# Kernel tuning notes

Hardware: AMD Instinct MI355X
Metric: run time of the kernel (lower is better)

## Reference

```python
import jax, jax.numpy as jnp
import numpy as np

NUM_HEADS = 8

def setup_inputs() -> dict:
    key = jax.random.key(0)
    ks = jax.random.split(key, 12)
    T, B, C, D = 2048, 4, 512, 512
    s = 1.0 / np.sqrt(C)
    return {
        "key_in": jax.random.normal(ks[0], (T, B, C), jnp.float32),
        "value_in": jax.random.normal(ks[1], (T, B, C), jnp.float32),
        "query_in": jax.random.normal(ks[2], (T, B, C), jnp.float32),
        "Wk": jax.random.normal(ks[3], (C, D), jnp.float32) * s,
        "bk": jax.random.normal(ks[4], (D,), jnp.float32) * 0.01,
        "Wv": jax.random.normal(ks[5], (C, D), jnp.float32) * s,
        "bv": jax.random.normal(ks[6], (D,), jnp.float32) * 0.01,
        "Wq": jax.random.normal(ks[7], (C, D), jnp.float32) * s,
        "bq": jax.random.normal(ks[8], (D,), jnp.float32) * 0.01,
        "Wo": jax.random.normal(ks[9], (D, D), jnp.float32) * (1.0 / np.sqrt(D)),
        "bo": jax.random.normal(ks[10], (D,), jnp.float32) * 0.01,
    }

def reference(key_in, value_in, query_in, Wk, bk, Wv, bv, Wq, bq, Wo, bo):
    T, B, C = query_in.shape
    D = Wq.shape[1]
    H = NUM_HEADS
    hd = D // H
    scale = 1.0 / np.sqrt(hd).astype(np.float32)
    # Linear projections on (T, B, C) -> (T, B, D), then the original's
    # row-major view(B, -1, H, hd) followed by transpose(1, 2) -> (B, H, T, hd)
    def proj(x, W, b):
        y = x @ W + b                      # (T, B, D)
        return y.reshape(B, -1, H, hd).transpose(0, 2, 1, 3)  # (B, H, T, hd)
    q = proj(query_in, Wq, bq)
    k = proj(key_in, Wk, bk)
    v = proj(value_in, Wv, bv)
    scores = jnp.einsum("bhqd,bhkd->bhqk", q, k) * scale  # (B, H, T, T)
    attn = jax.nn.softmax(scores, axis=-1)
    x = jnp.einsum("bhqk,bhkd->bhqd", attn, v)            # (B, H, T, hd)
    x = x.transpose(0, 2, 1, 3).reshape(T, B, D)          # matches .view(T, B, d_model)
    return x @ Wo + bo
```

## Files before the change

kernel.cpp:

```cpp
#include <hip/hip_runtime.h>
#include <math.h>

#define MROWS 8192
#define DM    512
#define SEQL  2048
#define HDIM  64
#define NSPLIT 2

typedef __attribute__((ext_vector_type(4))) float floatx4;
typedef _Float16 half2v __attribute__((ext_vector_type(2)));
typedef _Float16 half4v __attribute__((ext_vector_type(4)));
typedef _Float16 half8v __attribute__((ext_vector_type(8)));

#define CEXP 0.18033688011f

__device__ __forceinline__ void gll16(const void* g, void* l) {
    __builtin_amdgcn_global_load_lds(
        (const __attribute__((address_space(1))) unsigned int*)g,
        (__attribute__((address_space(3))) unsigned int*)l, 16, 0, 0);
}

__device__ __forceinline__ half4v pack4(float a, float b, float c, float d) {
    half2v lo = __builtin_bit_cast(half2v, __builtin_amdgcn_cvt_pkrtz(a, b));
    half2v hi = __builtin_bit_cast(half2v, __builtin_amdgcn_cvt_pkrtz(c, d));
    half4v r;
    r[0] = lo[0]; r[1] = lo[1]; r[2] = hi[0]; r[3] = hi[1];
    return r;
}

__global__ __launch_bounds__(256) void cast3(const float* __restrict__ s0,
                                             const float* __restrict__ s1,
                                             const float* __restrict__ s2,
                                             _Float16* __restrict__ d0,
                                             _Float16* __restrict__ d1,
                                             _Float16* __restrict__ d2) {
    const float* s = blockIdx.z == 0 ? s0 : (blockIdx.z == 1 ? s1 : s2);
    _Float16* d = blockIdx.z == 0 ? d0 : (blockIdx.z == 1 ? d1 : d2);
    const size_t i = ((size_t)blockIdx.x * 256 + threadIdx.x) * 8;
    const float4 f0 = *(const float4*)&s[i];
    const float4 f1 = *(const float4*)&s[i + 4];
    half8v o;
    o[0] = (_Float16)f0.x; o[1] = (_Float16)f0.y; o[2] = (_Float16)f0.z; o[3] = (_Float16)f0.w;
    o[4] = (_Float16)f1.x; o[5] = (_Float16)f1.y; o[6] = (_Float16)f1.z; o[7] = (_Float16)f1.w;
    *(half8v*)&d[i] = o;
}

__global__ __launch_bounds__(256) void transw(const float* __restrict__ w0,
                                              const float* __restrict__ w1,
                                              const float* __restrict__ w2,
                                              const float* __restrict__ w3,
                                              _Float16* __restrict__ t0,
                                              _Float16* __restrict__ t1,
                                              _Float16* __restrict__ t2,
                                              _Float16* __restrict__ t3) {
    __shared__ float tile[32][33];
    const float* W = blockIdx.z == 0 ? w0 : (blockIdx.z == 1 ? w1 : (blockIdx.z == 2 ? w2 : w3));
    _Float16* T = blockIdx.z == 0 ? t0 : (blockIdx.z == 1 ? t1 : (blockIdx.z == 2 ? t2 : t3));
    const float sc = (blockIdx.z == 0) ? CEXP : 1.0f;
    const int tx = threadIdx.x & 31, ty = threadIdx.x >> 5;
    const int x = blockIdx.x * 32 + tx;
    const int y0 = blockIdx.y * 32;
#pragma unroll
    for (int i = 0; i < 4; ++i)
        tile[ty + i * 8][tx] = W[(size_t)(y0 + ty + i * 8) * DM + x];
    __syncthreads();
    const int xo = y0 + tx;
#pragma unroll
    for (int i = 0; i < 4; ++i)
        T[(size_t)(blockIdx.x * 32 + ty + i * 8) * DM + xo] = (_Float16)(tile[tx][ty + i * 8] * sc);
}

__global__ __launch_bounds__(256, 3) void gemm_f16(
        const _Float16* __restrict__ A0, const _Float16* __restrict__ A1, const _Float16* __restrict__ A2,
        const _Float16* __restrict__ B0, const _Float16* __restrict__ B1, const _Float16* __restrict__ B2,
        const float* __restrict__ c0, const float* __restrict__ c1, const float* __restrict__ c2,
        void* __restrict__ o0, void* __restrict__ o1, void* __restrict__ o2,
        int modes, float bscale0) {
    __shared__ _Float16 As[128 * 64];
    __shared__ _Float16 Bs[64 * 64];
    const int z = blockIdx.z;
    const _Float16* A  = z == 0 ? A0 : (z == 1 ? A1 : A2);
    const _Float16* Bt = z == 0 ? B0 : (z == 1 ? B1 : B2);
    const float* bias  = z == 0 ? c0 : (z == 1 ? c1 : c2);
    void* outp         = z == 0 ? o0 : (z == 1 ? o1 : o2);
    const int mode = (modes >> (z * 4)) & 15;
    const float bscale = (z == 0) ? bscale0 : 1.0f;

    const int tid = threadIdx.x;
    const int w = tid >> 6;
    const int l15 = tid & 15, quad = (tid & 63) >> 4;
    const int n0 = blockIdx.x * 64, m0 = blockIdx.y * 128;

    floatx4 acc[2][4];
#pragma unroll
    for (int i = 0; i < 2; ++i)
#pragma unroll
        for (int j = 0; j < 4; ++j) acc[i][j] = (floatx4){0.f, 0.f, 0.f, 0.f};

    for (int kt = 0; kt < DM / 64; ++kt) {
        __syncthreads();
#pragma unroll
        for (int i = 0; i < 4; ++i) {
            const int c = i * 256 + tid;
            const int row = c >> 3, g = c & 7;
            const int kg = g ^ (row & 7);
            gll16(&A[(size_t)(m0 + row) * DM + kt * 64 + kg * 8], &As[c * 8]);
        }
#pragma unroll
        for (int i = 0; i < 2; ++i) {
            const int c = i * 256 + tid;
            const int row = c >> 3, g = c & 7;
            const int kg = g ^ (row & 7);
            gll16(&Bt[(size_t)(n0 + row) * DM + kt * 64 + kg * 8], &Bs[c * 8]);
        }
        __syncthreads();
#pragma unroll
        for (int ks = 0; ks < 2; ++ks) {
            half8v af[2], bfr[4];
#pragma unroll
            for (int i = 0; i < 2; ++i) {
                const int row = w * 32 + i * 16 + l15;
                af[i] = *(const half8v*)&As[row * 64 + ((ks * 4 + quad) ^ (row & 7)) * 8];
            }
#pragma unroll
            for (int j = 0; j < 4; ++j) {
                const int row = j * 16 + l15;
                bfr[j] = *(const half8v*)&Bs[row * 64 + ((ks * 4 + quad) ^ (row & 7)) * 8];
            }
#pragma unroll
            for (int i = 0; i < 2; ++i)
#pragma unroll
                for (int j = 0; j < 4; ++j)
                    acc[i][j] = __builtin_amdgcn_mfma_f32_16x16x32_f16(af[i], bfr[j], acc[i][j], 0, 0, 0);
        }
    }
#pragma unroll
    for (int j = 0; j < 4; ++j) {
        const int col = n0 + j * 16 + l15;
        const float bv = bias[col] * bscale;
#pragma unroll
        for (int i = 0; i < 2; ++i) {
            const int rb = m0 + w * 32 + i * 16 + quad * 4;
            if (mode == 2) {
                float* of = (float*)outp;
#pragma unroll
                for (int r = 0; r < 4; ++r)
                    of[(size_t)(rb + r) * DM + col] = acc[i][j][r] + bv;
            } else if (mode == 0) {
                _Float16* oh = (_Float16*)outp;
#pragma unroll
                for (int r = 0; r < 4; ++r)
                    oh[(size_t)(rb + r) * DM + col] = (_Float16)(acc[i][j][r] + bv);
            } else {
                _Float16* oh = (_Float16*)outp;
                const int g = rb >> 11, seq = rb & 2047;
                half4v pv;
#pragma unroll
                for (int r = 0; r < 4; ++r) pv[r] = (_Float16)(acc[i][j][r] + bv);
                *(half4v*)&oh[((size_t)g * DM + col) * SEQL + seq] = pv;
            }
        }
    }
}

__global__ __launch_bounds__(256, 4) void attn_mfma(const _Float16* __restrict__ Q16,
                                                    const _Float16* __restrict__ K16,
                                                    const _Float16* __restrict__ Vt,
                                                    _Float16* __restrict__ Opart,
                                                    float* __restrict__ lpart) {
    __shared__ _Float16 Ks[2][64 * 64];
    __shared__ _Float16 Vs[2][64 * 64];

    const int tid  = threadIdx.x;
    const int lane = tid & 63;
    const int l15  = lane & 15;
    const int quad = lane >> 4;

    const int pair  = blockIdx.y;
    const int split = blockIdx.z;
    const int grp   = pair >> 3;
    const int h     = pair & 7;
    const int q0    = blockIdx.x * 128;
    const int rQ    = grp * SEQL + q0 + (tid >> 6) * 32;
    const int cb    = h * HDIM;
    const int NIT   = (SEQL / 64) / NSPLIT;
    const int kt0   = split * NIT;

    const _Float16* Kbase = K16 + (size_t)grp * SEQL * DM + cb;
    const _Float16* Vbase = Vt + (size_t)grp * DM * SEQL + (size_t)cb * SEQL;

    half8v qf[2][2];
#pragma unroll
    for (int qt = 0; qt < 2; ++qt)
#pragma unroll
        for (int ks = 0; ks < 2; ++ks)
            qf[qt][ks] = *(const half8v*)&Q16[(size_t)(rQ + qt * 16 + l15) * DM + cb + ks * 32 + quad * 8];

    floatx4 oacc[2][4], lacc[2];
#pragma unroll
    for (int qt = 0; qt < 2; ++qt) {
        lacc[qt] = (floatx4){0.f, 0.f, 0.f, 0.f};
#pragma unroll
        for (int dt = 0; dt < 4; ++dt) oacc[qt][dt] = (floatx4){0.f, 0.f, 0.f, 0.f};
    }
    half4v ones;
    ones[0] = (_Float16)1.f; ones[1] = (_Float16)1.f; ones[2] = (_Float16)1.f; ones[3] = (_Float16)1.f;

#define STAGE(KT, B)                                                            \
    {                                                                           \
        _Float16* ksb = &Ks[B][0];                                              \
        _Float16* vsb = &Vs[B][0];                                              \
        _Pragma("unroll")                                                       \
        for (int i_ = 0; i_ < 4; ++i_) {                                        \
            const int c_ = i_ * 256 + tid;                                      \
            if (c_ < 512) {                                                     \
                const int key_ = c_ >> 3, g_ = c_ & 7;                          \
                const int dg_ = g_ ^ (key_ & 7);                                \
                gll16(&Kbase[(size_t)((KT) * 64 + key_) * DM + dg_ * 8],        \
                      &ksb[c_ * 8]);                                            \
            } else {                                                            \
                const int cv_ = c_ - 512;                                       \
                const int d_ = cv_ >> 3, g_ = cv_ & 7;                          \
                const int kg_ = g_ ^ (d_ & 7);                                  \
                gll16(&Vbase[(size_t)d_ * SEQL + (KT) * 64 + kg_ * 8],          \
                      &vsb[cv_ * 8]);                                           \
            }                                                                   \
        }                                                                       \
    }

    STAGE(kt0, 0)

    for (int it = 0; it < NIT; ++it) {
        const int cur = it & 1;
        __syncthreads();
        if (it + 1 < NIT) STAGE(kt0 + it + 1, cur ^ 1)

        const _Float16* ksb = &Ks[cur][0];
        const _Float16* vsb = &Vs[cur][0];

        floatx4 st[4][2];
#pragma unroll
        for (int ktile = 0; ktile < 4; ++ktile) {
            const int key = ktile * 16 + l15;
            const half8v kf0 = *(const half8v*)&ksb[key * 64 + ((0 + quad) ^ (key & 7)) * 8];
            const half8v kf1 = *(const half8v*)&ksb[key * 64 + ((4 + quad) ^ (key & 7)) * 8];
#pragma unroll
            for (int qt = 0; qt < 2; ++qt) {
                floatx4 z = {0.f, 0.f, 0.f, 0.f};
                z = __builtin_amdgcn_mfma_f32_16x16x32_f16(kf0, qf[qt][0], z, 0, 0, 0);
                st[ktile][qt] = __builtin_amdgcn_mfma_f32_16x16x32_f16(kf1, qf[qt][1], z, 0, 0, 0);
            }
        }

        half4v pa[4][2];
#pragma unroll
        for (int ktile = 0; ktile < 4; ++ktile)
#pragma unroll
            for (int qt = 0; qt < 2; ++qt)
                pa[ktile][qt] = pack4(__builtin_amdgcn_exp2f(st[ktile][qt][0]),
                                      __builtin_amdgcn_exp2f(st[ktile][qt][1]),
                                      __builtin_amdgcn_exp2f(st[ktile][qt][2]),
                                      __builtin_amdgcn_exp2f(st[ktile][qt][3]));

#pragma unroll
        for (int qt = 0; qt < 2; ++qt)
#pragma unroll
            for (int ktile = 0; ktile < 4; ++ktile)
                lacc[qt] = __builtin_amdgcn_mfma_f32_16x16x16f16(pa[ktile][qt], ones, lacc[qt], 0, 0, 0);

#pragma unroll
        for (int dt = 0; dt < 4; ++dt) {
            const int d = dt * 16 + l15;
#pragma unroll
            for (int ktile = 0; ktile < 4; ++ktile) {
                const int G = ktile * 2 + (quad >> 1);
                const int slot = G ^ (d & 7);
                const half4v vf = *(const half4v*)&vsb[d * 64 + slot * 8 + (quad & 1) * 4];
#pragma unroll
                for (int qt = 0; qt < 2; ++qt)
                    oacc[qt][dt] = __builtin_amdgcn_mfma_f32_16x16x16f16(pa[ktile][qt], vf, oacc[qt][dt], 0, 0, 0);
            }
        }
    }

    _Float16* Op = Opart + (size_t)split * MROWS * DM;
#pragma unroll
    for (int qt = 0; qt < 2; ++qt)
#pragma unroll
        for (int r = 0; r < 4; ++r) {
            const int qrow = rQ + qt * 16 + quad * 4 + r;
            const size_t rowoff = (size_t)qrow * DM + cb;
#pragma unroll
            for (int dt = 0; dt < 4; ++dt)
                Op[rowoff + dt * 16 + l15] = (_Float16)oacc[qt][dt][r];
            if (l15 == 0)
                lpart[((size_t)split * MROWS + qrow) * 8 + h] = lacc[qt][r];
        }
}

__global__ __launch_bounds__(256) void combine(const _Float16* __restrict__ Opart,
                                               const float* __restrict__ lpart,
                                               _Float16* __restrict__ O16) {
    const size_t idx = (size_t)blockIdx.x * 256 + threadIdx.x;
    const int row = idx >> 6;
    const int c8 = (idx & 63) * 8;
    const int h = c8 >> 6;
    const float l = lpart[(size_t)row * 8 + h] + lpart[((size_t)MROWS + row) * 8 + h];
    const float inv = 1.0f / l;
    const half8v a = *(const half8v*)&Opart[(size_t)row * DM + c8];
    const half8v b = *(const half8v*)&Opart[(size_t)MROWS * DM + (size_t)row * DM + c8];
    half8v o;
#pragma unroll
    for (int i = 0; i < 8; ++i)
        o[i] = (_Float16)(((float)a[i] + (float)b[i]) * inv);
    *(half8v*)&O16[(size_t)row * DM + c8] = o;
}

extern "C" void kernel_launch(void* const* d_in, const int* in_sizes, int n_in,
                              void* d_out, int out_size, void* d_ws, size_t ws_size,
                              hipStream_t stream) {
    const float* key_in   = (const float*)d_in[0];
    const float* value_in = (const float*)d_in[1];
    const float* query_in = (const float*)d_in[2];
    const float* Wk = (const float*)d_in[3];
    const float* bk = (const float*)d_in[4];
    const float* Wv = (const float*)d_in[5];
    const float* bv = (const float*)d_in[6];
    const float* Wq = (const float*)d_in[7];
    const float* bq = (const float*)d_in[8];
    const float* Wo = (const float*)d_in[9];
    const float* bo = (const float*)d_in[10];
    float* out = (float*)d_out;

    const size_t MAT = (size_t)MROWS * DM;
    _Float16* Xq16 = (_Float16*)d_ws;
    _Float16* Xk16 = Xq16 + MAT;
    _Float16* Xv16 = Xk16 + MAT;
    _Float16* Q16  = Xv16 + MAT;
    _Float16* K16  = Q16 + MAT;
    _Float16* Vtb  = K16 + MAT;
    _Float16* Wqt  = Vtb + MAT;
    _Float16* Wkt  = Wqt + DM * DM;
    _Float16* Wvt  = Wkt + DM * DM;
    _Float16* Wot  = Wvt + DM * DM;
    float*    lpart = (float*)(Wot + DM * DM);
    _Float16* Opart = Xq16;
    _Float16* O16   = Xv16;

    const dim3 blk(256);

    cast3<<<dim3(2048, 1, 3), blk, 0, stream>>>(query_in, key_in, value_in, Xq16, Xk16, Xv16);
    transw<<<dim3(16, 16, 4), blk, 0, stream>>>(Wq, Wk, Wv, Wo, Wqt, Wkt, Wvt, Wot);

    gemm_f16<<<dim3(DM / 64, MROWS / 128, 3), blk, 0, stream>>>(
        Xq16, Xk16, Xv16, Wqt, Wkt, Wvt, bq, bk, bv,
        (void*)Q16, (void*)K16, (void*)Vtb, 0 | (0 << 4) | (1 << 8), CEXP);

    attn_mfma<<<dim3(SEQL / 128, 32, NSPLIT), blk, 0, stream>>>(Q16, K16, Vtb, Opart, lpart);
    combine<<<dim3(MROWS * DM / 8 / 256), blk, 0, stream>>>(Opart, lpart, O16);

    gemm_f16<<<dim3(DM / 64, MROWS / 128, 1), blk, 0, stream>>>(
        O16, O16, O16, Wot, Wot, Wot, bo, bo, bo,
        (void*)out, (void*)out, (void*)out, 2, 1.0f);
}
```

Measured before the change: 213.6 us.

## Fuse input cast into projection GEMM and split-combine into output GEMM

Removes the standalone fp32-to-fp16 cast kernel by converting activations inside the projection GEMM's A-tile load. Removes the combine kernel by merging the two split partials and normalizing by the softmax denominators while loading A tiles in the output GEMM. Both GEMMs are retiled: the projection GEMM keeps the full 512-wide weight panel in LDS with 32-row M tiles, and the output GEMM uses 256-wide N tiles. This saves two launches and the fp16 intermediate round trips, at the cost of synchronous, non-async A loads, re-streaming the weights for every small M tile, and lower parallelism per block.

New measurement: 201.6 us. -5.6%, faster.

```diff
diff --git a/kernel.cpp b/kernel.cpp
--- a/kernel.cpp
+++ b/kernel.cpp
@@ -26,23 +26,6 @@
     half4v r;
     r[0] = lo[0]; r[1] = lo[1]; r[2] = hi[0]; r[3] = hi[1];
     return r;
-}
-
-__global__ __launch_bounds__(256) void cast3(const float* __restrict__ s0,
-                                             const float* __restrict__ s1,
-                                             const float* __restrict__ s2,
-                                             _Float16* __restrict__ d0,
-                                             _Float16* __restrict__ d1,
-                                             _Float16* __restrict__ d2) {
-    const float* s = blockIdx.z == 0 ? s0 : (blockIdx.z == 1 ? s1 : s2);
-    _Float16* d = blockIdx.z == 0 ? d0 : (blockIdx.z == 1 ? d1 : d2);
-    const size_t i = ((size_t)blockIdx.x * 256 + threadIdx.x) * 8;
-    const float4 f0 = *(const float4*)&s[i];
-    const float4 f1 = *(const float4*)&s[i + 4];
-    half8v o;
-    o[0] = (_Float16)f0.x; o[1] = (_Float16)f0.y; o[2] = (_Float16)f0.z; o[3] = (_Float16)f0.w;
-    o[4] = (_Float16)f1.x; o[5] = (_Float16)f1.y; o[6] = (_Float16)f1.z; o[7] = (_Float16)f1.w;
-    *(half8v*)&d[i] = o;
 }
 
 __global__ __launch_bounds__(256) void transw(const float* __restrict__ w0,
@@ -70,26 +53,103 @@
         T[(size_t)(blockIdx.x * 32 + ty + i * 8) * DM + xo] = (_Float16)(tile[tx][ty + i * 8] * sc);
 }
 
-__global__ __launch_bounds__(256, 3) void gemm_f16(
-        const _Float16* __restrict__ A0, const _Float16* __restrict__ A1, const _Float16* __restrict__ A2,
-        const _Float16* __restrict__ B0, const _Float16* __restrict__ B1, const _Float16* __restrict__ B2,
-        const float* __restrict__ c0, const float* __restrict__ c1, const float* __restrict__ c2,
-        void* __restrict__ o0, void* __restrict__ o1, void* __restrict__ o2,
-        int modes, float bscale0) {
-    __shared__ _Float16 As[128 * 64];
-    __shared__ _Float16 Bs[64 * 64];
-    const int z = blockIdx.z;
-    const _Float16* A  = z == 0 ? A0 : (z == 1 ? A1 : A2);
-    const _Float16* Bt = z == 0 ? B0 : (z == 1 ? B1 : B2);
-    const float* bias  = z == 0 ? c0 : (z == 1 ? c1 : c2);
-    void* outp         = z == 0 ? o0 : (z == 1 ? o1 : o2);
-    const int mode = (modes >> (z * 4)) & 15;
-    const float bscale = (z == 0) ? bscale0 : 1.0f;
+__global__ __launch_bounds__(256, 3) void proj_gemm(
+        const float* __restrict__ q32, const float* __restrict__ k32, const float* __restrict__ v32,
+        const _Float16* __restrict__ Wq, const _Float16* __restrict__ Wk, const _Float16* __restrict__ Wv,
+        const float* __restrict__ bq, const float* __restrict__ bk, const float* __restrict__ bv,
+        _Float16* __restrict__ Qo, _Float16* __restrict__ Ko, _Float16* __restrict__ Vto) {
+    __shared__ _Float16 Bs[512 * 32];
+    __shared__ _Float16 As[32 * 32];
+    const int z = blockIdx.y;
+    const float* A32    = z == 0 ? q32 : (z == 1 ? k32 : v32);
+    const _Float16* Bt  = z == 0 ? Wq : (z == 1 ? Wk : Wv);
+    const float* bias   = z == 0 ? bq : (z == 1 ? bk : bv);
+    const float bscale  = z == 0 ? CEXP : 1.0f;
 
     const int tid = threadIdx.x;
     const int w = tid >> 6;
     const int l15 = tid & 15, quad = (tid & 63) >> 4;
-    const int n0 = blockIdx.x * 64, m0 = blockIdx.y * 128;
+    const int m0 = blockIdx.x * 32;
+
+    floatx4 acc[2][8];
+#pragma unroll
+    for (int i = 0; i < 2; ++i)
+#pragma unroll
+        for (int j = 0; j < 8; ++j) acc[i][j] = (floatx4){0.f, 0.f, 0.f, 0.f};
+
+    for (int kt = 0; kt < DM / 32; ++kt) {
+        __syncthreads();
+#pragma unroll
+        for (int i = 0; i < 8; ++i) {
+            const int c = i * 256 + tid;
+            const int row = c >> 2, g = c & 3;
+            const int kg = g ^ (row & 3);
+            gll16(&Bt[(size_t)row * DM + kt * 32 + kg * 8], &Bs[c * 8]);
+        }
+        if (tid < 128) {
+            const int c = tid;
+            const int row = c >> 2, g = c & 3;
+            const int kg = g ^ (row & 3);
+            const float* src = &A32[(size_t)(m0 + row) * DM + kt * 32 + kg * 8];
+            const float4 f0 = *(const float4*)&src[0];
+            const float4 f1 = *(const float4*)&src[4];
+            half8v o;
+            o[0] = (_Float16)f0.x; o[1] = (_Float16)f0.y; o[2] = (_Float16)f0.z; o[3] = (_Float16)f0.w;
+            o[4] = (_Float16)f1.x; o[5] = (_Float16)f1.y; o[6] = (_Float16)f1.z; o[7] = (_Float16)f1.w;
+            *(half8v*)&As[c * 8] = o;
+        }
+        __syncthreads();
+        half8v af[2], bfr[8];
+#pragma unroll
+        for (int i = 0; i < 2; ++i) {
+            const int row = i * 16 + l15;
+            af[i] = *(const half8v*)&As[row * 32 + (quad ^ (row & 3)) * 8];
+        }
+#pragma unroll
+        for (int j = 0; j < 8; ++j) {
+            const int row = w * 128 + j * 16 + l15;
+            bfr[j] = *(const half8v*)&Bs[row * 32 + (quad ^ (row & 3)) * 8];
+        }
+#pragma unroll
+        for (int i = 0; i < 2; ++i)
+#pragma unroll
+            for (int j = 0; j < 8; ++j)
+                acc[i][j] = __builtin_amdgcn_mfma_f32_16x16x32_f16(af[i], bfr[j], acc[i][j], 0, 0, 0);
+    }
+#pragma unroll
+    for (int j = 0; j < 8; ++j) {
+        const int col = w * 128 + j * 16 + l15;
+        const float bv4 = bias[col] * bscale;
+#pragma unroll
+        for (int i = 0; i < 2; ++i) {
+            const int rb = m0 + i * 16 + quad * 4;
+            if (z == 2) {
+                const int g = rb >> 11, seq = rb & 2047;
+                half4v pv;
+#pragma unroll
+                for (int r = 0; r < 4; ++r) pv[r] = (_Float16)(acc[i][j][r] + bv4);
+                *(half4v*)&Vto[((size_t)g * DM + col) * SEQL + seq] = pv;
+            } else {
+                _Float16* oh = z == 0 ? Qo : Ko;
+#pragma unroll
+                for (int r = 0; r < 4; ++r)
+                    oh[(size_t)(rb + r) * DM + col] = (_Float16)(acc[i][j][r] + bv4);
+            }
+        }
+    }
+}
+
+__global__ __launch_bounds__(256, 4) void out_gemm(
+        const _Float16* __restrict__ Op0, const _Float16* __restrict__ Op1,
+        const float* __restrict__ lp,
+        const _Float16* __restrict__ Wo, const float* __restrict__ bo,
+        float* __restrict__ out) {
+    __shared__ _Float16 Bs[256 * 64];
+    __shared__ _Float16 As[32 * 64];
+    const int tid = threadIdx.x;
+    const int w = tid >> 6;
+    const int l15 = tid & 15, quad = (tid & 63) >> 4;
+    const int n0 = blockIdx.x * 256, m0 = blockIdx.y * 32;
 
     floatx4 acc[2][4];
 #pragma unroll
@@ -100,18 +160,27 @@
     for (int kt = 0; kt < DM / 64; ++kt) {
         __syncthreads();
 #pragma unroll
-        for (int i = 0; i < 4; ++i) {
+        for (int i = 0; i < 8; ++i) {
             const int c = i * 256 + tid;
             const int row = c >> 3, g = c & 7;
             const int kg = g ^ (row & 7);
-            gll16(&A[(size_t)(m0 + row) * DM + kt * 64 + kg * 8], &As[c * 8]);
-        }
-#pragma unroll
-        for (int i = 0; i < 2; ++i) {
-            const int c = i * 256 + tid;
+            gll16(&Wo[(size_t)(n0 + row) * DM + kt * 64 + kg * 8], &Bs[c * 8]);
+        }
+        {
+            const int c = tid;
             const int row = c >> 3, g = c & 7;
             const int kg = g ^ (row & 7);
-            gll16(&Bt[(size_t)(n0 + row) * DM + kt * 64 + kg * 8], &Bs[c * 8]);
+            const int grow = m0 + row;
+            const size_t off = (size_t)grow * DM + kt * 64 + kg * 8;
+            const half8v a = *(const half8v*)&Op0[off];
+            const half8v b = *(const half8v*)&Op1[off];
+            const float inv = 1.0f / (lp[(size_t)grow * 8 + kt] +
+                                      lp[((size_t)MROWS + grow) * 8 + kt]);
+            half8v s;
+#pragma unroll
+            for (int e = 0; e < 8; ++e)
+                s[e] = (_Float16)(((float)a[e] + (float)b[e]) * inv);
+            *(half8v*)&As[c * 8] = s;
         }
         __syncthreads();
 #pragma unroll
@@ -119,12 +188,12 @@
             half8v af[2], bfr[4];
 #pragma unroll
             for (int i = 0; i < 2; ++i) {
-                const int row = w * 32 + i * 16 + l15;
+                const int row = i * 16 + l15;
                 af[i] = *(const half8v*)&As[row * 64 + ((ks * 4 + quad) ^ (row & 7)) * 8];
             }
 #pragma unroll
             for (int j = 0; j < 4; ++j) {
-                const int row = j * 16 + l15;
+                const int row = w * 64 + j * 16 + l15;
                 bfr[j] = *(const half8v*)&Bs[row * 64 + ((ks * 4 + quad) ^ (row & 7)) * 8];
             }
 #pragma unroll
@@ -136,29 +205,14 @@
     }
 #pragma unroll
     for (int j = 0; j < 4; ++j) {
-        const int col = n0 + j * 16 + l15;
-        const float bv = bias[col] * bscale;
+        const int col = n0 + w * 64 + j * 16 + l15;
+        const float bv4 = bo[col];
 #pragma unroll
         for (int i = 0; i < 2; ++i) {
-            const int rb = m0 + w * 32 + i * 16 + quad * 4;
-            if (mode == 2) {
-                float* of = (float*)outp;
-#pragma unroll
-                for (int r = 0; r < 4; ++r)
-                    of[(size_t)(rb + r) * DM + col] = acc[i][j][r] + bv;
-            } else if (mode == 0) {
-                _Float16* oh = (_Float16*)outp;
-#pragma unroll
-                for (int r = 0; r < 4; ++r)
-                    oh[(size_t)(rb + r) * DM + col] = (_Float16)(acc[i][j][r] + bv);
-            } else {
-                _Float16* oh = (_Float16*)outp;
-                const int g = rb >> 11, seq = rb & 2047;
-                half4v pv;
-#pragma unroll
-                for (int r = 0; r < 4; ++r) pv[r] = (_Float16)(acc[i][j][r] + bv);
-                *(half4v*)&oh[((size_t)g * DM + col) * SEQL + seq] = pv;
-            }
+            const int rb = m0 + i * 16 + quad * 4;
+#pragma unroll
+            for (int r = 0; r < 4; ++r)
+                out[(size_t)(rb + r) * DM + col] = acc[i][j][r] + bv4;
         }
     }
 }
@@ -298,24 +352,6 @@
         }
 }
 
-__global__ __launch_bounds__(256) void combine(const _Float16* __restrict__ Opart,
-                                               const float* __restrict__ lpart,
-                                               _Float16* __restrict__ O16) {
-    const size_t idx = (size_t)blockIdx.x * 256 + threadIdx.x;
-    const int row = idx >> 6;
-    const int c8 = (idx & 63) * 8;
-    const int h = c8 >> 6;
-    const float l = lpart[(size_t)row * 8 + h] + lpart[((size_t)MROWS + row) * 8 + h];
-    const float inv = 1.0f / l;
-    const half8v a = *(const half8v*)&Opart[(size_t)row * DM + c8];
-    const half8v b = *(const half8v*)&Opart[(size_t)MROWS * DM + (size_t)row * DM + c8];
-    half8v o;
-#pragma unroll
-    for (int i = 0; i < 8; ++i)
-        o[i] = (_Float16)(((float)a[i] + (float)b[i]) * inv);
-    *(half8v*)&O16[(size_t)row * DM + c8] = o;
-}
-
 extern "C" void kernel_launch(void* const* d_in, const int* in_sizes, int n_in,
                               void* d_out, int out_size, void* d_ws, size_t ws_size,
                               hipStream_t stream) {
@@ -333,10 +369,7 @@
     float* out = (float*)d_out;
 
     const size_t MAT = (size_t)MROWS * DM;
-    _Float16* Xq16 = (_Float16*)d_ws;
-    _Float16* Xk16 = Xq16 + MAT;
-    _Float16* Xv16 = Xk16 + MAT;
-    _Float16* Q16  = Xv16 + MAT;
+    _Float16* Q16  = (_Float16*)d_ws;
     _Float16* K16  = Q16 + MAT;
     _Float16* Vtb  = K16 + MAT;
     _Float16* Wqt  = Vtb + MAT;
@@ -344,22 +377,17 @@
     _Float16* Wvt  = Wkt + DM * DM;
     _Float16* Wot  = Wvt + DM * DM;
     float*    lpart = (float*)(Wot + DM * DM);
-    _Float16* Opart = Xq16;
-    _Float16* O16   = Xv16;
+    _Float16* Opart = (_Float16*)(lpart + 2 * MROWS * 8);
 
     const dim3 blk(256);
 
-    cast3<<<dim3(2048, 1, 3), blk, 0, stream>>>(query_in, key_in, value_in, Xq16, Xk16, Xv16);
     transw<<<dim3(16, 16, 4), blk, 0, stream>>>(Wq, Wk, Wv, Wo, Wqt, Wkt, Wvt, Wot);
 
-    gemm_f16<<<dim3(DM / 64, MROWS / 128, 3), blk, 0, stream>>>(
-        Xq16, Xk16, Xv16, Wqt, Wkt, Wvt, bq, bk, bv,
-        (void*)Q16, (void*)K16, (void*)Vtb, 0 | (0 << 4) | (1 << 8), CEXP);
+    proj_gemm<<<dim3(MROWS / 32, 3), blk, 0, stream>>>(
+        query_in, key_in, value_in, Wqt, Wkt, Wvt, bq, bk, bv, Q16, K16, Vtb);
 
     attn_mfma<<<dim3(SEQL / 128, 32, NSPLIT), blk, 0, stream>>>(Q16, K16, Vtb, Opart, lpart);
-    combine<<<dim3(MROWS * DM / 8 / 256), blk, 0, stream>>>(Opart, lpart, O16);
-
-    gemm_f16<<<dim3(DM / 64, MROWS / 128, 1), blk, 0, stream>>>(
-        O16, O16, O16, Wot, Wot, Wot, bo, bo, bo,
-        (void*)out, (void*)out, (void*)out, 2, 1.0f);
-}
+
+    out_gemm<<<dim3(2, MROWS / 32), blk, 0, stream>>>(
+        Opart, Opart + MAT, lpart, Wot, bo, out);
+}
```
